# Optimization experiments

Measured on AMD Instinct MI355X. Metric: run time of the kernel, lower is better.

## Reference

```python
import jax, jax.numpy as jnp
import numpy as np
import math

B, NU, NA = 8, 256, 256
USER_DIM, ANT_DIM, EDGE_DIM = 128, 128, 64
HIDDEN, HEADS = 512, 8
HEAD_DIM = HIDDEN // HEADS  # 64
SLOPE = 0.2


def setup_inputs() -> dict:
    key = jax.random.key(0)
    ks = jax.random.split(key, 8)
    s = 0.05
    return {
        "user_feats": jax.random.normal(ks[0], (B, NU, USER_DIM), jnp.float32),
        "ant_feats": jax.random.normal(ks[1], (B, NA, ANT_DIM), jnp.float32),
        "edge_feats": jax.random.normal(ks[2], (B, NU, NA, EDGE_DIM), jnp.float32),
        # per-head projection weights, stored as [H, in_dim, head_dim] for x @ W
        "Wu": jax.random.normal(ks[3], (HEADS, USER_DIM, HEAD_DIM), jnp.float32) * s,
        "Wa": jax.random.normal(ks[4], (HEADS, ANT_DIM, HEAD_DIM), jnp.float32) * s,
        "We": jax.random.normal(ks[5], (HEADS, EDGE_DIM, HEAD_DIM), jnp.float32) * s,
        "av": jax.random.normal(ks[6], (HEADS, HEAD_DIM), jnp.float32) * s,
        "Wres": jax.random.normal(ks[7], (USER_DIM, HIDDEN), jnp.float32) * s,
    }


def reference(user_feats, ant_feats, edge_feats, Wu, Wa, We, av, Wres):
    scale = 1.0 / math.sqrt(HEAD_DIM)
    user_heads, ant_heads = [], []
    # loop over fixed small number of heads (mirrors module structure),
    # keeps the large [B,NU,NA,HEAD_DIM] intermediate to one head at a time
    for k in range(HEADS):
        U = user_feats @ Wu[k]          # [B,NU,hd]
        A = ant_feats @ Wa[k]           # [B,NA,hd]
        E = jnp.einsum('bune,ed->bund', edge_feats, We[k])  # [B,NU,NA,hd]
        S = U[:, :, None, :] + A[:, None, :, :] + E          # [B,NU,NA,hd]
        act = jnp.where(S >= 0, S, SLOPE * S)                # leaky relu 0.2
        score = jnp.einsum('bund,d->bun', act, av[k]) * scale
        alpha = jax.nn.softmax(score, axis=-1)               # over antennas
        # dropout p=0.3 is identity in eval mode
        aw = alpha[..., None]
        user_heads.append(((A[:, None, :, :] + E) * aw).sum(axis=2))  # [B,NU,hd]
        ant_heads.append(((U[:, :, None, :] + E) * aw).sum(axis=1))   # [B,NA,hd]
    user_out = jnp.concatenate(user_heads, axis=-1) + user_feats @ Wres
    ant_out = jnp.concatenate(ant_heads, axis=-1)
    return (user_out, ant_out)
```

## Files before the change

### kernel.cpp

```cpp
#include <hip/hip_runtime.h>
#include <math.h>

constexpr int B_  = 8;
constexpr int NU  = 256;
constexpr int NA  = 256;
constexpr int UD  = 128;
constexpr int ED  = 64;
constexpr int H   = 8;
constexpr int HD  = 64;
constexpr int HID = 512;
constexpr float SLOPE = 0.2f;
constexpr float SCALE = 0.125f;

constexpr size_t WS_UT    = 0;
constexpr size_t WS_AT    = 1048576;
constexpr size_t WS_UBASE = 2097152;
constexpr size_t WS_ALPHA = 3145728;
constexpr size_t WS_WET32 = 7340032;
constexpr size_t WS_WET16 = 7372800;

typedef __attribute__((ext_vector_type(8))) short short8v;
typedef __attribute__((ext_vector_type(4))) float f32x4;

static __device__ __forceinline__ unsigned short f2bf(float f) {
  unsigned int u = __float_as_uint(f);
  unsigned int r = (u + 0x7fffu + ((u >> 16) & 1u)) >> 16;
  return (unsigned short)r;
}

static __device__ __forceinline__ void block_sync_lds() {
  asm volatile("s_waitcnt lgkmcnt(0)" ::: "memory");
  __builtin_amdgcn_sched_barrier(0);
  __builtin_amdgcn_s_barrier();
  __builtin_amdgcn_sched_barrier(0);
}

__global__ __launch_bounds__(256) void prep_kernel(
    const float* __restrict__ user, const float* __restrict__ ant,
    const float* __restrict__ Wu, const float* __restrict__ Wa,
    const float* __restrict__ Wres, float* __restrict__ ws)
{
  const int job = blockIdx.y;
  const int r0  = blockIdx.x * 4;
  const int b   = r0 >> 8, lr = r0 & 255;
  const int t   = threadIdx.x;

  const float* X = (job == 1) ? ant : user;
  const float* W = (job == 0) ? Wu : (job == 1) ? Wa : Wres;

  __shared__ float xs[4][UD];
  #pragma unroll
  for (int i = 0; i < 2; ++i) {
    int idx = i * 256 + t;
    xs[idx >> 7][idx & 127] = X[(size_t)(r0 + (idx >> 7)) * UD + (idx & 127)];
  }
  __syncthreads();

  const int j0 = 2 * t;
  const float* wp;
  int wstride;
  if (job < 2) { wp = W + (size_t)(j0 >> 6) * (UD * HD) + (j0 & 63); wstride = HD; }
  else         { wp = W + j0;                                        wstride = HID; }

  float2 acc[4];
  #pragma unroll
  for (int r = 0; r < 4; ++r) acc[r] = make_float2(0.f, 0.f);

  for (int k = 0; k < UD; ++k) {
    float2 w = *(const float2*)(wp + (size_t)k * wstride);
    #pragma unroll
    for (int r = 0; r < 4; ++r) {
      float x = xs[r][k];
      acc[r].x += x * w.x;
      acc[r].y += x * w.y;
    }
  }

  if (job < 2) {
    float* T = ws + (job == 0 ? WS_UT : WS_AT);
    float4 w0 = make_float4(acc[0].x, acc[1].x, acc[2].x, acc[3].x);
    float4 w1 = make_float4(acc[0].y, acc[1].y, acc[2].y, acc[3].y);
    *(float4*)(T + ((size_t)b * HID + j0)     * 256 + lr) = w0;
    *(float4*)(T + ((size_t)b * HID + j0 + 1) * 256 + lr) = w1;
  } else {
    float* outp = ws + WS_UBASE;
    #pragma unroll
    for (int r = 0; r < 4; ++r)
      *(float2*)(outp + (size_t)(r0 + r) * HID + j0) = acc[r];
  }
}

__global__ __launch_bounds__(256) void weprep_kernel(
    const float* __restrict__ We, float* __restrict__ ws)
{
  const int h = blockIdx.x;
  const int t = threadIdx.x;
  __shared__ float lds[ED * HD];

  const float4* src = (const float4*)(We + (size_t)h * ED * HD);
  #pragma unroll
  for (int i = 0; i < 4; ++i) ((float4*)lds)[i * 256 + t] = src[i * 256 + t];
  __syncthreads();

  const int d = t >> 2, q = t & 3;
  float* WeTf = ws + WS_WET32;
  unsigned short* WeT16 = (unsigned short*)(ws + WS_WET16);
  const size_t jrow = (size_t)(h * HD + d) * ED;
  #pragma unroll
  for (int k = 0; k < 16; ++k) {
    const int e = q * 16 + k;
    float v = lds[e * HD + d];
    WeTf[jrow + e]  = v;
    WeT16[jrow + e] = f2bf(v);
  }
}

__global__ __launch_bounds__(512, 4) void score_user_kernel(
    const float* __restrict__ edge, const float* __restrict__ av,
    float* __restrict__ ws, float* __restrict__ out)
{
  const int bid = blockIdx.x;
  const int b = bid >> 8, u = bid & 255;
  const int t = threadIdx.x;

  __shared__ __align__(16) short ebuf[2][32 * ED];
  __shared__ float sc[NA * 9];
  __shared__ float gu[HID];
  __shared__ float sinv[H];

  const float* UT = ws + WS_UT;
  const float* AT = ws + WS_AT;

  const int w    = t >> 6;
  const int lane = t & 63;
  const int l16  = lane & 15;
  const int kgrp = lane >> 4;

  short8v wf[4][2];
  float   ucol[4];
  float   avv[4];
  const unsigned short* WeT16 = (const unsigned short*)(ws + WS_WET16);
  #pragma unroll
  for (int n = 0; n < 4; ++n) {
    const int j = 64 * w + 16 * n + l16;
    #pragma unroll
    for (int c = 0; c < 2; ++c)
      wf[n][c] = *(const short8v*)(WeT16 + (size_t)j * ED + c * 32 + kgrp * 8);
    ucol[n] = UT[((size_t)b * HID + j) * 256 + u];
    avv[n]  = av[j] * SCALE;
  }

  const float4* ep = (const float4*)(edge + (size_t)bid * NA * ED);
  const int srow = t >> 4, sc4 = t & 15;
  const int sbyte = (srow * 128 + sc4 * 8) ^ ((srow & 7) << 4);
  float4 v = ep[t];

  const float* ATbase = AT + (size_t)b * HID * 256 + kgrp * 4;

  float lsum = 0.f;
  float O[4] = {0.f, 0.f, 0.f, 0.f};

  for (int t8 = 0; t8 < 8; ++t8) {
    const int cur = t8 & 1;
    {
      ushort4 bv = make_ushort4(f2bf(v.x), f2bf(v.y), f2bf(v.z), f2bf(v.w));
      *(ushort4*)((char*)ebuf[cur] + sbyte) = bv;
    }
    if (t8 < 7) v = ep[(t8 + 1) * 512 + t];

    const int a0 = t8 * 32;
    f32x4 acc[2][4];
    #pragma unroll
    for (int m = 0; m < 2; ++m)
      #pragma unroll
      for (int n = 0; n < 4; ++n) {
        const int j = 64 * w + 16 * n + l16;
        float4 a4 = *(const float4*)(ATbase + (size_t)j * 256 + a0 + m * 16);
        f32x4 vv; vv[0] = a4.x; vv[1] = a4.y; vv[2] = a4.z; vv[3] = a4.w;
        acc[m][n] = vv;
      }

    block_sync_lds();

    short8v af[2][2];
    #pragma unroll
    for (int m = 0; m < 2; ++m) {
      #pragma unroll
      for (int c = 0; c < 2; ++c) {
        int row = m * 16 + l16;
        int byte = (row * 128 + (c * 32 + kgrp * 8) * 2) ^ ((row & 7) << 4);
        af[m][c] = *(const short8v*)((const char*)ebuf[cur] + byte);
      }
    }

    #pragma unroll
    for (int c = 0; c < 2; ++c)
      #pragma unroll
      for (int m = 0; m < 2; ++m)
        #pragma unroll
        for (int n = 0; n < 4; ++n)
          acc[m][n] = __builtin_amdgcn_mfma_f32_16x16x32_bf16(
              af[m][c], wf[n][c], acc[m][n], 0, 0, 0);

    #pragma unroll
    for (int m = 0; m < 2; ++m) {
      #pragma unroll
      for (int q = 0; q < 4; ++q) {
        float h0 = 0.f;
        #pragma unroll
        for (int n = 0; n < 4; ++n) {
          float s = acc[m][n][q] + ucol[n];
          float sl = fmaxf(s, 0.f) + SLOPE * fminf(s, 0.f);
          h0 = fmaf(sl, avv[n], h0);
        }
        #pragma unroll
        for (int off = 8; off >= 1; off >>= 1) h0 += __shfl_xor(h0, off);
        float e = __expf(h0);
        lsum += e;
        if (l16 == 0) sc[(a0 + m * 16 + kgrp * 4 + q) * 9 + w] = e;
        #pragma unroll
        for (int n = 0; n < 4; ++n) O[n] += e * acc[m][n][q];
      }
    }
  }

  lsum += __shfl_xor(lsum, 16);
  lsum += __shfl_xor(lsum, 32);
  #pragma unroll
  for (int n = 0; n < 4; ++n) {
    O[n] += __shfl_xor(O[n], 16);
    O[n] += __shfl_xor(O[n], 32);
  }
  const float inv = 1.0f / lsum;

  if (lane == 0) sinv[w] = inv;
  if (kgrp == 0) {
    #pragma unroll
    for (int n = 0; n < 4; ++n) gu[w * 64 + n * 16 + l16] = O[n] * inv;
  }
  __syncthreads();

  {
    float* ag = ws + WS_ALPHA;
    #pragma unroll
    for (int i = 0; i < 4; ++i) {
      int idx = i * 512 + t;
      int a = idx >> 3, hh = idx & 7;
      ag[(((size_t)b * NA + a) * NU + u) * H + hh] = sc[a * 9 + hh] * sinv[hh];
    }
  }
  out[(size_t)bid * HID + t] = gu[t] + ws[WS_UBASE + (size_t)bid * HID + t];
}

__global__ __launch_bounds__(512, 4) void ant_kernel(
    const float* __restrict__ edge, float* __restrict__ ws,
    float* __restrict__ out)
{
  const int bid = blockIdx.x;
  const int b = bid >> 6, a0 = (bid & 63) * 4;
  const int t = threadIdx.x;
  const int w = t >> 6;
  const int lane = t & 63;

  __shared__ float plds[NU * 36];
  __shared__ float galds[4 * H * ED];

  {
    const float4* ag = (const float4*)(ws + WS_ALPHA + ((size_t)b * NA + a0) * NU * H);
    #pragma unroll
    for (int r = 0; r < 4; ++r) {
      int idx4 = r * 512 + t;
      int a = idx4 >> 9, rem = idx4 & 511;
      int uu = rem >> 1, hq = rem & 1;
      float4 vv = ag[idx4];
      float* dst = plds + uu * 36 + hq * 16 + a;
      dst[0]  = vv.x;
      dst[4]  = vv.y;
      dst[8]  = vv.z;
      dst[12] = vv.w;
    }
  }
  __syncthreads();

  const int u_loc = lane >> 4, e4 = lane & 15;
  float4 g[4] = {{0,0,0,0},{0,0,0,0},{0,0,0,0},{0,0,0,0}};

  {
    const float* ebase0 = edge + (((size_t)b * NU) * NA + a0) * ED + e4 * 4;
    for (int u0 = 0; u0 < NU; u0 += 4) {
      const int uu = u0 + u_loc;
      float4 p4 = *(const float4*)(plds + uu * 36 + w * 4);
      const float* ebase = ebase0 + (size_t)uu * (NA * ED);
      float4 e0 = *(const float4*)(ebase);
      float4 e1 = *(const float4*)(ebase + ED);
      float4 e2 = *(const float4*)(ebase + 2 * ED);
      float4 e3 = *(const float4*)(ebase + 3 * ED);
      g[0].x += p4.x * e0.x; g[0].y += p4.x * e0.y; g[0].z += p4.x * e0.z; g[0].w += p4.x * e0.w;
      g[1].x += p4.y * e1.x; g[1].y += p4.y * e1.y; g[1].z += p4.y * e1.z; g[1].w += p4.y * e1.w;
      g[2].x += p4.z * e2.x; g[2].y += p4.z * e2.y; g[2].z += p4.z * e2.z; g[2].w += p4.z * e2.w;
      g[3].x += p4.w * e3.x; g[3].y += p4.w * e3.y; g[3].z += p4.w * e3.z; g[3].w += p4.w * e3.w;
    }
  }
  #pragma unroll
  for (int al = 0; al < 4; ++al) {
    g[al].x += __shfl_xor(g[al].x, 16); g[al].x += __shfl_xor(g[al].x, 32);
    g[al].y += __shfl_xor(g[al].y, 16); g[al].y += __shfl_xor(g[al].y, 32);
    g[al].z += __shfl_xor(g[al].z, 16); g[al].z += __shfl_xor(g[al].z, 32);
    g[al].w += __shfl_xor(g[al].w, 16); g[al].w += __shfl_xor(g[al].w, 32);
  }
  if (u_loc == 0) {
    #pragma unroll
    for (int al = 0; al < 4; ++al)
      *(float4*)(galds + (al * H + w) * ED + e4 * 4) = g[al];
  }

  float pu[4] = {0.f, 0.f, 0.f, 0.f};
  {
    const float* UTj = ws + WS_UT + ((size_t)b * HID + t) * 256;
    for (int u0 = 0; u0 < NU; u0 += 4) {
      float4 U4 = *(const float4*)(UTj + u0);
      float4 p0 = *(const float4*)(plds + (u0 + 0) * 36 + w * 4);
      float4 p1 = *(const float4*)(plds + (u0 + 1) * 36 + w * 4);
      float4 p2 = *(const float4*)(plds + (u0 + 2) * 36 + w * 4);
      float4 p3 = *(const float4*)(plds + (u0 + 3) * 36 + w * 4);
      pu[0] += p0.x*U4.x + p1.x*U4.y + p2.x*U4.z + p3.x*U4.w;
      pu[1] += p0.y*U4.x + p1.y*U4.y + p2.y*U4.z + p3.y*U4.w;
      pu[2] += p0.z*U4.x + p1.z*U4.y + p2.z*U4.z + p3.z*U4.w;
      pu[3] += p0.w*U4.x + p1.w*U4.y + p2.w*U4.z + p3.w*U4.w;
    }
  }
  __syncthreads();

  {
    const float* wrow = ws + WS_WET32 + (size_t)t * ED;
    float o[4] = {pu[0], pu[1], pu[2], pu[3]};
    for (int e0 = 0; e0 < ED; e0 += 4) {
      float4 wv = *(const float4*)(wrow + e0);
      #pragma unroll
      for (int al = 0; al < 4; ++al) {
        float4 ga4 = *(const float4*)(galds + (al * H + w) * ED + e0);
        o[al] += ga4.x*wv.x + ga4.y*wv.y + ga4.z*wv.z + ga4.w*wv.w;
      }
    }
    float* outa = out + (size_t)(B_ * NU) * HID;
    #pragma unroll
    for (int al = 0; al < 4; ++al)
      outa[(size_t)((b * NA) + a0 + al) * HID + t] = o[al];
  }
}

extern "C" void kernel_launch(void* const* d_in, const int* in_sizes, int n_in,
                              void* d_out, int out_size, void* d_ws, size_t ws_size,
                              hipStream_t stream) {
  const float* user = (const float*)d_in[0];
  const float* ant  = (const float*)d_in[1];
  const float* edge = (const float*)d_in[2];
  const float* Wu   = (const float*)d_in[3];
  const float* Wa   = (const float*)d_in[4];
  const float* We   = (const float*)d_in[5];
  const float* av   = (const float*)d_in[6];
  const float* Wres = (const float*)d_in[7];
  float* out = (float*)d_out;
  float* ws  = (float*)d_ws;

  prep_kernel<<<dim3(512, 3), 256, 0, stream>>>(user, ant, Wu, Wa, Wres, ws);
  weprep_kernel<<<dim3(8), 256, 0, stream>>>(We, ws);
  score_user_kernel<<<dim3(B_ * NU), 512, 0, stream>>>(edge, av, ws, out);
  ant_kernel<<<dim3(B_ * 64), 512, 0, stream>>>(edge, ws, out);
}
```

Before: 275.5 us.

## Transpose MFMA operands in score_user kernel and store A row-major

The antenna projection A is now written row-major ([b,a,hid]) instead of transposed, and the score kernel swaps MFMA operand order so the output dimension lies along the accumulator's register axis. Each tile now covers 16 antennas instead of 32, which means 16 iterations instead of 8 and a smaller LDS edge buffer. This lets each lane fold the leaky-relu dot product in registers with only two cross-lane shuffles per tile instead of four per row. The costs are 16 output accumulators per lane, a 4-step shuffle reduction at the end, and twice as many block barriers.

```diff
diff --git a/kernel.cpp b/kernel.cpp
--- a/kernel.cpp
+++ b/kernel.cpp
@@ -13,7 +13,7 @@
 constexpr float SCALE = 0.125f;
 
 constexpr size_t WS_UT    = 0;
-constexpr size_t WS_AT    = 1048576;
+constexpr size_t WS_AROW  = 1048576;
 constexpr size_t WS_UBASE = 2097152;
 constexpr size_t WS_ALPHA = 3145728;
 constexpr size_t WS_WET32 = 7340032;
@@ -76,14 +76,14 @@
     }
   }
 
-  if (job < 2) {
-    float* T = ws + (job == 0 ? WS_UT : WS_AT);
+  if (job == 0) {
+    float* T = ws + WS_UT;
     float4 w0 = make_float4(acc[0].x, acc[1].x, acc[2].x, acc[3].x);
     float4 w1 = make_float4(acc[0].y, acc[1].y, acc[2].y, acc[3].y);
     *(float4*)(T + ((size_t)b * HID + j0)     * 256 + lr) = w0;
     *(float4*)(T + ((size_t)b * HID + j0 + 1) * 256 + lr) = w1;
   } else {
-    float* outp = ws + WS_UBASE;
+    float* outp = ws + (job == 1 ? WS_AROW : WS_UBASE);
     #pragma unroll
     for (int r = 0; r < 4; ++r)
       *(float2*)(outp + (size_t)(r0 + r) * HID + j0) = acc[r];
@@ -123,13 +123,13 @@
   const int b = bid >> 8, u = bid & 255;
   const int t = threadIdx.x;
 
-  __shared__ __align__(16) short ebuf[2][32 * ED];
+  __shared__ __align__(16) short ebuf[2][16 * ED];
   __shared__ float sc[NA * 9];
   __shared__ float gu[HID];
   __shared__ float sinv[H];
 
-  const float* UT = ws + WS_UT;
-  const float* AT = ws + WS_AT;
+  const float* UT   = ws + WS_UT;
+  const float* Aall = ws + WS_AROW;
 
   const int w    = t >> 6;
   const int lane = t & 63;
@@ -137,106 +137,112 @@
   const int kgrp = lane >> 4;
 
   short8v wf[4][2];
-  float   ucol[4];
-  float   avv[4];
+  float u16[16], av16[16];
   const unsigned short* WeT16 = (const unsigned short*)(ws + WS_WET16);
   #pragma unroll
-  for (int n = 0; n < 4; ++n) {
-    const int j = 64 * w + 16 * n + l16;
+  for (int jm = 0; jm < 4; ++jm) {
+    const int jf = 64 * w + 16 * jm + l16;
     #pragma unroll
     for (int c = 0; c < 2; ++c)
-      wf[n][c] = *(const short8v*)(WeT16 + (size_t)j * ED + c * 32 + kgrp * 8);
-    ucol[n] = UT[((size_t)b * HID + j) * 256 + u];
-    avv[n]  = av[j] * SCALE;
-  }
-
-  const float4* ep = (const float4*)(edge + (size_t)bid * NA * ED);
-  const int srow = t >> 4, sc4 = t & 15;
-  const int sbyte = (srow * 128 + sc4 * 8) ^ ((srow & 7) << 4);
-  float4 v = ep[t];
-
-  const float* ATbase = AT + (size_t)b * HID * 256 + kgrp * 4;
+      wf[jm][c] = *(const short8v*)(WeT16 + (size_t)jf * ED + c * 32 + kgrp * 8);
+    #pragma unroll
+    for (int q = 0; q < 4; ++q) {
+      const int j = 64 * w + 16 * jm + kgrp * 4 + q;
+      u16[jm * 4 + q]  = UT[((size_t)b * HID + j) * 256 + u];
+      av16[jm * 4 + q] = av[j] * SCALE;
+    }
+  }
+
+  const float2* ep2 = (const float2*)(edge + (size_t)bid * NA * ED);
+  const int srow = t >> 5, sc2 = t & 31;
+  const int swrbyte = (srow * 128 + sc2 * 4) ^ ((srow & 7) << 4);
+  float2 v = ep2[t];
 
   float lsum = 0.f;
-  float O[4] = {0.f, 0.f, 0.f, 0.f};
-
-  for (int t8 = 0; t8 < 8; ++t8) {
-    const int cur = t8 & 1;
+  float O[16];
+  #pragma unroll
+  for (int i = 0; i < 16; ++i) O[i] = 0.f;
+
+  for (int tile = 0; tile < 16; ++tile) {
+    const int cur = tile & 1;
     {
-      ushort4 bv = make_ushort4(f2bf(v.x), f2bf(v.y), f2bf(v.z), f2bf(v.w));
-      *(ushort4*)((char*)ebuf[cur] + sbyte) = bv;
-    }
-    if (t8 < 7) v = ep[(t8 + 1) * 512 + t];
-
-    const int a0 = t8 * 32;
-    f32x4 acc[2][4];
-    #pragma unroll
-    for (int m = 0; m < 2; ++m)
-      #pragma unroll
-      for (int n = 0; n < 4; ++n) {
-        const int j = 64 * w + 16 * n + l16;
-        float4 a4 = *(const float4*)(ATbase + (size_t)j * 256 + a0 + m * 16);
+      unsigned int pk = (unsigned int)f2bf(v.x) | ((unsigned int)f2bf(v.y) << 16);
+      *(unsigned int*)((char*)ebuf[cur] + swrbyte) = pk;
+    }
+    if (tile < 15) v = ep2[(tile + 1) * 512 + t];
+
+    const int arow = tile * 16 + l16;
+    f32x4 acc[4];
+    {
+      const float* Arow = Aall + ((size_t)(b * NA + arow)) * HID + 64 * w + kgrp * 4;
+      #pragma unroll
+      for (int jm = 0; jm < 4; ++jm) {
+        float4 a4 = *(const float4*)(Arow + jm * 16);
         f32x4 vv; vv[0] = a4.x; vv[1] = a4.y; vv[2] = a4.z; vv[3] = a4.w;
-        acc[m][n] = vv;
+        acc[jm] = vv;
       }
+    }
 
     block_sync_lds();
 
-    short8v af[2][2];
-    #pragma unroll
-    for (int m = 0; m < 2; ++m) {
-      #pragma unroll
-      for (int c = 0; c < 2; ++c) {
-        int row = m * 16 + l16;
-        int byte = (row * 128 + (c * 32 + kgrp * 8) * 2) ^ ((row & 7) << 4);
-        af[m][c] = *(const short8v*)((const char*)ebuf[cur] + byte);
+    short8v af[2];
+    #pragma unroll
+    for (int c = 0; c < 2; ++c) {
+      int byte = (l16 * 128 + c * 64 + kgrp * 16) ^ ((l16 & 7) << 4);
+      af[c] = *(const short8v*)((const char*)ebuf[cur] + byte);
+    }
+
+    #pragma unroll
+    for (int c = 0; c < 2; ++c)
+      #pragma unroll
+      for (int jm = 0; jm < 4; ++jm)
+        acc[jm] = __builtin_amdgcn_mfma_f32_16x16x32_bf16(
+            wf[jm][c], af[c], acc[jm], 0, 0, 0);
+
+    float p0 = 0.f, p1 = 0.f;
+    #pragma unroll
+    for (int jm = 0; jm < 4; ++jm) {
+      #pragma unroll
+      for (int q = 0; q < 4; ++q) {
+        float s = acc[jm][q] + u16[jm * 4 + q];
+        float sl = fmaxf(s, 0.f) + SLOPE * fminf(s, 0.f);
+        if (((q) & 1) == 0) p0 = fmaf(sl, av16[jm * 4 + q], p0);
+        else                p1 = fmaf(sl, av16[jm * 4 + q], p1);
       }
     }
-
-    #pragma unroll
-    for (int c = 0; c < 2; ++c)
-      #pragma unroll
-      for (int m = 0; m < 2; ++m)
-        #pragma unroll
-        for (int n = 0; n < 4; ++n)
-          acc[m][n] = __builtin_amdgcn_mfma_f32_16x16x32_bf16(
-              af[m][c], wf[n][c], acc[m][n], 0, 0, 0);
-
-    #pragma unroll
-    for (int m = 0; m < 2; ++m) {
-      #pragma unroll
-      for (int q = 0; q < 4; ++q) {
-        float h0 = 0.f;
-        #pragma unroll
-        for (int n = 0; n < 4; ++n) {
-          float s = acc[m][n][q] + ucol[n];
-          float sl = fmaxf(s, 0.f) + SLOPE * fminf(s, 0.f);
-          h0 = fmaf(sl, avv[n], h0);
-        }
-        #pragma unroll
-        for (int off = 8; off >= 1; off >>= 1) h0 += __shfl_xor(h0, off);
-        float e = __expf(h0);
-        lsum += e;
-        if (l16 == 0) sc[(a0 + m * 16 + kgrp * 4 + q) * 9 + w] = e;
-        #pragma unroll
-        for (int n = 0; n < 4; ++n) O[n] += e * acc[m][n][q];
-      }
-    }
-  }
-
-  lsum += __shfl_xor(lsum, 16);
-  lsum += __shfl_xor(lsum, 32);
-  #pragma unroll
-  for (int n = 0; n < 4; ++n) {
-    O[n] += __shfl_xor(O[n], 16);
-    O[n] += __shfl_xor(O[n], 32);
-  }
+    float p = p0 + p1;
+    p += __shfl_xor(p, 16);
+    p += __shfl_xor(p, 32);
+    float e = __expf(p);
+    lsum += e;
+    if (kgrp == 0) sc[arow * 9 + w] = e;
+    #pragma unroll
+    for (int jm = 0; jm < 4; ++jm)
+      #pragma unroll
+      for (int q = 0; q < 4; ++q)
+        O[jm * 4 + q] = fmaf(e, acc[jm][q], O[jm * 4 + q]);
+  }
+
+  #pragma unroll
+  for (int i = 0; i < 16; ++i) {
+    O[i] += __shfl_xor(O[i], 1);
+    O[i] += __shfl_xor(O[i], 2);
+    O[i] += __shfl_xor(O[i], 4);
+    O[i] += __shfl_xor(O[i], 8);
+  }
+  lsum += __shfl_xor(lsum, 1);
+  lsum += __shfl_xor(lsum, 2);
+  lsum += __shfl_xor(lsum, 4);
+  lsum += __shfl_xor(lsum, 8);
   const float inv = 1.0f / lsum;
 
   if (lane == 0) sinv[w] = inv;
-  if (kgrp == 0) {
-    #pragma unroll
-    for (int n = 0; n < 4; ++n) gu[w * 64 + n * 16 + l16] = O[n] * inv;
+  if (l16 == 0) {
+    #pragma unroll
+    for (int jm = 0; jm < 4; ++jm)
+      #pragma unroll
+      for (int q = 0; q < 4; ++q)
+        gu[64 * w + 16 * jm + kgrp * 4 + q] = O[jm * 4 + q] * inv;
   }
   __syncthreads();
 
```

After: 391.2 us. +42.0%, slower.
